# Performance work log

Hardware: AMD Instinct MI355X
Metric: run time of the kernel (lower is better)

## Reference

```python
import jax, jax.numpy as jnp
import numpy as np

B, C, D = 32768, 1000, 512
ALPHA, BETA = 1.0, 1.0
TEMPERATURE = 0.1


def setup_inputs() -> dict:
    key = jax.random.key(0)
    k1, k2, k3, k4 = jax.random.split(key, 4)
    return {
        "features_front": jax.random.normal(k1, (B, D), dtype=jnp.float32),
        "logits": jax.random.normal(k2, (B, C), dtype=jnp.float32),
        "labels": jax.random.randint(k3, (B,), 0, C, dtype=jnp.int64),
        "text_prototype": jax.random.normal(k4, (C, D), dtype=jnp.float32),
    }


def reference(features_front, logits, labels, text_prototype):
    num_class = text_prototype.shape[0]

    # F.cross_entropy (mean reduction)
    logp = jax.nn.log_softmax(logits, axis=-1)
    loss_ce = -jnp.mean(jnp.take_along_axis(logp, labels[:, None], axis=1)[:, 0])

    # F.normalize(prototypes, dim=1)
    norm = jnp.linalg.norm(text_prototype, axis=1, keepdims=True)
    prototypes = text_prototype / jnp.maximum(norm, 1e-12)

    # supervised contrastive term against class prototypes
    feat_dot_prototype = (features_front @ prototypes.T) / TEMPERATURE  # [B, C]
    logits_max = jax.lax.stop_gradient(jnp.max(feat_dot_prototype, axis=1, keepdims=True))
    lg = feat_dot_prototype - logits_max
    log_prob = lg - jnp.log(jnp.sum(jnp.exp(lg), axis=1, keepdims=True))
    mask = (labels[:, None] == jnp.arange(num_class)[None, :]).astype(log_prob.dtype)
    mean_log_prob_pos = jnp.sum(mask * log_prob, axis=1)
    simloss = -jnp.mean(mean_log_prob_pos)

    # prototype repulsion: sum_{i != j} exp(p_i . p_j) == masked exp-sum of Gram matrix
    gram = prototypes @ prototypes.T  # [C, C]
    offdiag = 1.0 - jnp.eye(num_class, dtype=gram.dtype)
    textloss = jnp.log(jnp.sum(jnp.exp(gram) * offdiag)) / num_class

    return ALPHA * simloss + BETA * loss_ce + textloss
```

## Files before the change

### kernel.cpp

```cpp
#include <hip/hip_runtime.h>
#include <math.h>

#define NB 32768
#define NC 1000
#define ND 512
#define NTILES 63
#define LOG2E 1.4426950408889634f
#define LN2 0.6931471805599453f
#define S2 14.426950408889634f
#define NBUCKET 64

typedef __attribute__((ext_vector_type(8))) short short8;
typedef __attribute__((ext_vector_type(4))) float f32x4;

__device__ __forceinline__ float fexp2(float x) {
    float r; asm("v_exp_f32 %0, %1" : "=v"(r) : "v"(x)); return r;
}
__device__ __forceinline__ float flog2(float x) {
    float r; asm("v_log_f32 %0, %1" : "=v"(r) : "v"(x)); return r;
}
__device__ __forceinline__ unsigned short bf16_rne(float f) {
    unsigned int u = __builtin_bit_cast(unsigned int, f);
    u += 0x7FFFu + ((u >> 16) & 1u);
    return (unsigned short)(u >> 16);
}
__device__ __forceinline__ short8 pack8f(float4 a, float4 b) {
    short8 s;
    s[0] = (short)bf16_rne(a.x); s[1] = (short)bf16_rne(a.y);
    s[2] = (short)bf16_rne(a.z); s[3] = (short)bf16_rne(a.w);
    s[4] = (short)bf16_rne(b.x); s[5] = (short)bf16_rne(b.y);
    s[6] = (short)bf16_rne(b.z); s[7] = (short)bf16_rne(b.w);
    return s;
}

__global__ __launch_bounds__(256) void norm_protos(const float* __restrict__ pro,
                                                   unsigned short* __restrict__ pbf) {
    const int row = blockIdx.x, t = threadIdx.x;
    const int tile = row >> 4, r = row & 15;
    const int kk = t >> 4, g = (t >> 2) & 3, slot = t & 3;
    unsigned int* dst = (unsigned int*)pbf +
        ((size_t)tile * 1024 + kk * 64 + g * 16 + r) * 4 + slot;
    if (row >= NC) { *dst = 0u; return; }
    const float* rp = pro + (size_t)row * ND;
    const float x0 = rp[2 * t], x1 = rp[2 * t + 1];
    float ss = x0 * x0 + x1 * x1;
#pragma unroll
    for (int o = 1; o < 64; o <<= 1) ss += __shfl_xor(ss, o, 64);
    __shared__ float part[4];
    if ((t & 63) == 0) part[t >> 6] = ss;
    __syncthreads();
    const float nrm = sqrtf(part[0] + part[1] + part[2] + part[3]);
    const float sc = 1.0f / fmaxf(nrm, 1e-12f);
    *dst = (unsigned int)bf16_rne(x0 * sc) | ((unsigned int)bf16_rne(x1 * sc) << 16);
}

__global__ __launch_bounds__(256, 3) void fat_kernel(const float* __restrict__ feat,
                                                     const float* __restrict__ logits,
                                                     const int* __restrict__ labels,
                                                     const unsigned short* __restrict__ pbf,
                                                     float* __restrict__ buckets,
                                                     float4* __restrict__ part) {
    __shared__ short8 lds[2][1024];
    __shared__ float wsum[4];
    const int role = blockIdx.x % 3;
    const int idx = blockIdx.x / 3;
    const int t = threadIdx.x;
    const int wid = t >> 6, lane = t & 63;
    const short8* frag = (const short8*)pbf;

    if (role == 0) {
        const int rb = idx >> 1, ch = idx & 1;
        const int t0 = ch ? 32 : 0;
        const int nt = ch ? 31 : 32;
        const int r16 = lane & 15, g = lane >> 4;
        const int rowbase = rb * 64 + wid * 16;

        {
            const short8* src = frag + t0 * 1024;
#pragma unroll
            for (int q = 0; q < 4; ++q) {
                const int id = t + 256 * q;
                __builtin_amdgcn_global_load_lds(
                    (const __attribute__((address_space(1))) unsigned int*)(src + id),
                    (__attribute__((address_space(3))) unsigned int*)(&lds[0][0] + id), 16, 0, 0);
            }
        }
        short8 bf[16];
        {
            const float* f0 = feat + (size_t)(rowbase + r16) * ND + 8 * g;
#pragma unroll
            for (int kk = 0; kk < 16; ++kk)
                bf[kk] = pack8f(*(const float4*)(f0 + 32 * kk), *(const float4*)(f0 + 32 * kk + 4));
        }
        int lab0 = labels[rowbase + r16];
        lab0 = lab0 < 0 ? 0 : (lab0 > NC - 1 ? NC - 1 : lab0);

        float m0 = -INFINITY, ls0 = 0.f, lv0 = 0.f;
        __syncthreads();

#pragma unroll 1
        for (int j = 0; j < nt; ++j) {
            const short8* cur = lds[j & 1];
            if (j + 1 < nt) {
                short8* nxt = lds[(j + 1) & 1];
                const short8* src = frag + (t0 + j + 1) * 1024;
#pragma unroll
                for (int q = 0; q < 4; ++q) {
                    const int id = t + 256 * q;
                    __builtin_amdgcn_global_load_lds(
                        (const __attribute__((address_space(1))) unsigned int*)(src + id),
                        (__attribute__((address_space(3))) unsigned int*)(nxt + id), 16, 0, 0);
                }
            }
            f32x4 aE = {0.f, 0.f, 0.f, 0.f}, aO = {0.f, 0.f, 0.f, 0.f};
#pragma unroll
            for (int kk = 0; kk < 8; ++kk) {
                aE = __builtin_amdgcn_mfma_f32_16x16x32_bf16(cur[kk * 64 + lane], bf[kk], aE, 0, 0, 0);
                aO = __builtin_amdgcn_mfma_f32_16x16x32_bf16(cur[(8 + kk) * 64 + lane], bf[8 + kk], aO, 0, 0, 0);
            }
            const int cbase = (t0 + j) * 16 + g * 4;
            float x[4];
#pragma unroll
            for (int rI = 0; rI < 4; ++rI) {
                const float v = (aE[rI] + aO[rI]) * S2;
                x[rI] = (cbase + rI < NC) ? v : -INFINITY;
                lv0 += (cbase + rI == lab0) ? v : 0.f;
            }
            const float tmax = fmaxf(fmaxf(x[0], x[1]), fmaxf(x[2], x[3]));
            const float mn = fmaxf(m0, tmax);
            ls0 *= fexp2(m0 - mn);
            m0 = mn;
            ls0 += fexp2(x[0] - mn) + fexp2(x[1] - mn) + fexp2(x[2] - mn) + fexp2(x[3] - mn);
            __syncthreads();
        }

#pragma unroll
        for (int o = 16; o <= 32; o <<= 1) {
            const float mo = __shfl_xor(m0, o, 64), lo = __shfl_xor(ls0, o, 64);
            lv0 += __shfl_xor(lv0, o, 64);
            const float mm = fmaxf(m0, mo);
            ls0 = ls0 * fexp2(m0 - mm) + lo * fexp2(mo - mm);
            m0 = mm;
        }
        if (lane < 16) {
            float4 p; p.x = m0; p.y = ls0; p.z = lv0; p.w = 0.f;
            part[(size_t)(rowbase + r16) * 2 + ch] = p;
        }

    } else if (role == 1) {
        const int rowbase = idx * 32 + wid * 8;
        const int q4 = lane >> 4, l16 = lane & 15;
        float localce = 0.f;
#pragma unroll 1
        for (int i = 0; i < 2; ++i) {
            const int row = rowbase + 4 * i + q4;
            const float* rp = logits + (size_t)row * NC;
            const float4* rp4 = (const float4*)rp;
            float4 xs[16];
#pragma unroll
            for (int j = 0; j < 15; ++j) {
                const float4 v = rp4[l16 + 16 * j];
                xs[j].x = v.x * LOG2E; xs[j].y = v.y * LOG2E;
                xs[j].z = v.z * LOG2E; xs[j].w = v.w * LOG2E;
            }
            if (l16 < 10) {
                const float4 v = rp4[l16 + 240];
                xs[15].x = v.x * LOG2E; xs[15].y = v.y * LOG2E;
                xs[15].z = v.z * LOG2E; xs[15].w = v.w * LOG2E;
            } else {
                xs[15].x = xs[15].y = xs[15].z = xs[15].w = -INFINITY;
            }
            float m = -INFINITY;
#pragma unroll
            for (int j = 0; j < 16; ++j)
                m = fmaxf(m, fmaxf(fmaxf(xs[j].x, xs[j].y), fmaxf(xs[j].z, xs[j].w)));
#pragma unroll
            for (int o = 1; o <= 8; o <<= 1) m = fmaxf(m, __shfl_xor(m, o, 64));
            float s = 0.f;
#pragma unroll
            for (int j = 0; j < 16; ++j)
                s += fexp2(xs[j].x - m) + fexp2(xs[j].y - m) +
                     fexp2(xs[j].z - m) + fexp2(xs[j].w - m);
#pragma unroll
            for (int o = 1; o <= 8; o <<= 1) s += __shfl_xor(s, o, 64);
            if (l16 == 0) {
                int lab = labels[row];
                lab = lab < 0 ? 0 : (lab > NC - 1 ? NC - 1 : lab);
                localce += (m + flog2(s)) * LN2 - rp[lab];
            }
        }
#pragma unroll
        for (int o = 1; o < 64; o <<= 1) localce += __shfl_xor(localce, o, 64);
        if (lane == 0) wsum[wid] = localce;
        __syncthreads();
        if (t == 0)
            atomicAdd(buckets + 1024 + (idx & (NBUCKET - 1)) * 16,
                      (wsum[0] + wsum[1] + wsum[2] + wsum[3]) * (1.0f / (float)NB));

    } else {
        if (idx >= 1008) return;
        const int ct = idx >> 4;
        const int bx = idx & 15;
        const int r16 = lane & 15, g = lane >> 4;
        const int btile = bx * 4 + wid;
        const int irow = btile * 16 + r16;

        short8 af[16], bfr[16];
#pragma unroll
        for (int kk = 0; kk < 16; ++kk) {
            af[kk] = frag[(size_t)ct * 1024 + kk * 64 + lane];
            bfr[kk] = frag[(size_t)btile * 1024 + kk * 64 + lane];
        }
        f32x4 dacc = {0.f, 0.f, 0.f, 0.f};
#pragma unroll
        for (int kk = 0; kk < 16; ++kk)
            dacc = __builtin_amdgcn_mfma_f32_16x16x32_bf16(af[kk], bfr[kk], dacc, 0, 0, 0);

        float s = 0.f;
        if (irow < NC) {
            const int cbase = ct * 16 + g * 4;
#pragma unroll
            for (int rI = 0; rI < 4; ++rI) {
                const int j = cbase + rI;
                if (j < NC && j != irow) s += fexp2(dacc[rI] * LOG2E);
            }
        }
#pragma unroll
        for (int o = 1; o < 64; o <<= 1) s += __shfl_xor(s, o, 64);
        if (lane == 0) wsum[wid] = s;
        __syncthreads();
        if (t == 0)
            atomicAdd(buckets + 2048 + (idx & (NBUCKET - 1)) * 16,
                      wsum[0] + wsum[1] + wsum[2] + wsum[3]);
    }
}

__global__ __launch_bounds__(256) void simmerge_kernel(const float4* __restrict__ part,
                                                       float* __restrict__ buckets) {
    __shared__ float wsum[4];
    const int t = threadIdx.x, wid = t >> 6, lane = t & 63;
    const int row = blockIdx.x * 256 + t;
    const float4 p0 = part[(size_t)row * 2];
    const float4 p1 = part[(size_t)row * 2 + 1];
    const float M = fmaxf(p0.x, p1.x);
    const float LS = p0.y * fexp2(p0.x - M) + p1.y * fexp2(p1.x - M);
    float v = (M + flog2(LS) - (p0.z + p1.z)) * LN2 * (1.0f / (float)NB);
#pragma unroll
    for (int o = 1; o < 64; o <<= 1) v += __shfl_xor(v, o, 64);
    if (lane == 0) wsum[wid] = v;
    __syncthreads();
    if (t == 0)
        atomicAdd(buckets + (blockIdx.x & (NBUCKET - 1)) * 16,
                  wsum[0] + wsum[1] + wsum[2] + wsum[3]);
}

__global__ void combine_kernel(const float* __restrict__ a, float* __restrict__ out) {
    const int t = threadIdx.x;
    float s = a[t * 16], c = a[1024 + t * 16], gr = a[2048 + t * 16];
#pragma unroll
    for (int o = 1; o < 64; o <<= 1) {
        s += __shfl_xor(s, o, 64);
        c += __shfl_xor(c, o, 64);
        gr += __shfl_xor(gr, o, 64);
    }
    if (t == 0) out[0] = s + c + logf(gr) * (1.0f / (float)NC);
}

extern "C" void kernel_launch(void* const* d_in, const int* in_sizes, int n_in,
                              void* d_out, int out_size, void* d_ws, size_t ws_size,
                              hipStream_t stream) {
    const float* feat   = (const float*)d_in[0];
    const float* logits = (const float*)d_in[1];
    const int*   labels = (const int*)d_in[2];
    const float* pro    = (const float*)d_in[3];
    float* out = (float*)d_out;

    float* acc = (float*)d_ws;
    unsigned short* pbf = (unsigned short*)((char*)d_ws + 16384);
    float4* part = (float4*)((char*)d_ws + (2u << 20));

    hipMemsetAsync(d_ws, 0, 3072 * sizeof(float), stream);
    hipLaunchKernelGGL(norm_protos,     dim3(1024), dim3(256), 0, stream, pro, pbf);
    hipLaunchKernelGGL(fat_kernel,      dim3(3072), dim3(256), 0, stream,
                       feat, logits, labels, pbf, acc, part);
    hipLaunchKernelGGL(simmerge_kernel, dim3(128),  dim3(256), 0, stream, part, acc);
    hipLaunchKernelGGL(combine_kernel,  dim3(1),    dim3(64),  0, stream, acc, out);
}
```

Measured before the change: 99.05 us.

## Double rows per wave in sim GEMM and rebalance block role mix

Each sim-role wave now processes two 16-row feature tiles against each staged prototype tile, reusing every LDS fragment for two MFMAs and halving the number of sim blocks. The block role split changes from thirds to fifths so the CE and Gram roles keep their counts, and the grid shrinks to match. The CE path folds the LOG2E scaling into an FMA inside the exp. Launch bounds drop to one block per SIMD target, which allows many more registers but may reduce occupancy and latency hiding.

```diff
diff --git a/kernel.cpp b/kernel.cpp
--- a/kernel.cpp
+++ b/kernel.cpp
@@ -54,7 +54,7 @@
     *dst = (unsigned int)bf16_rne(x0 * sc) | ((unsigned int)bf16_rne(x1 * sc) << 16);
 }
 
-__global__ __launch_bounds__(256, 3) void fat_kernel(const float* __restrict__ feat,
+__global__ __launch_bounds__(256, 1) void fat_kernel(const float* __restrict__ feat,
                                                      const float* __restrict__ logits,
                                                      const int* __restrict__ labels,
                                                      const unsigned short* __restrict__ pbf,
@@ -62,18 +62,19 @@
                                                      float4* __restrict__ part) {
     __shared__ short8 lds[2][1024];
     __shared__ float wsum[4];
-    const int role = blockIdx.x % 3;
-    const int idx = blockIdx.x / 3;
+    const int r5 = blockIdx.x % 5;
+    const int q5 = blockIdx.x / 5;
     const int t = threadIdx.x;
     const int wid = t >> 6, lane = t & 63;
     const short8* frag = (const short8*)pbf;
 
-    if (role == 0) {
+    if (r5 == 0) {
+        const int idx = q5;
         const int rb = idx >> 1, ch = idx & 1;
         const int t0 = ch ? 32 : 0;
         const int nt = ch ? 31 : 32;
         const int r16 = lane & 15, g = lane >> 4;
-        const int rowbase = rb * 64 + wid * 16;
+        const int rowbase = rb * 128 + wid * 32;
 
         {
             const short8* src = frag + t0 * 1024;
@@ -85,17 +86,23 @@
                     (__attribute__((address_space(3))) unsigned int*)(&lds[0][0] + id), 16, 0, 0);
             }
         }
-        short8 bf[16];
+        short8 bf0[16], bf1[16];
         {
             const float* f0 = feat + (size_t)(rowbase + r16) * ND + 8 * g;
-#pragma unroll
-            for (int kk = 0; kk < 16; ++kk)
-                bf[kk] = pack8f(*(const float4*)(f0 + 32 * kk), *(const float4*)(f0 + 32 * kk + 4));
+            const float* f1 = f0 + 16 * ND;
+#pragma unroll
+            for (int kk = 0; kk < 16; ++kk) {
+                bf0[kk] = pack8f(*(const float4*)(f0 + 32 * kk), *(const float4*)(f0 + 32 * kk + 4));
+                bf1[kk] = pack8f(*(const float4*)(f1 + 32 * kk), *(const float4*)(f1 + 32 * kk + 4));
+            }
         }
         int lab0 = labels[rowbase + r16];
+        int lab1 = labels[rowbase + 16 + r16];
         lab0 = lab0 < 0 ? 0 : (lab0 > NC - 1 ? NC - 1 : lab0);
+        lab1 = lab1 < 0 ? 0 : (lab1 > NC - 1 ? NC - 1 : lab1);
 
         float m0 = -INFINITY, ls0 = 0.f, lv0 = 0.f;
+        float m1 = -INFINITY, ls1 = 0.f, lv1 = 0.f;
         __syncthreads();
 
 #pragma unroll 1
@@ -112,42 +119,76 @@
                         (__attribute__((address_space(3))) unsigned int*)(nxt + id), 16, 0, 0);
                 }
             }
-            f32x4 aE = {0.f, 0.f, 0.f, 0.f}, aO = {0.f, 0.f, 0.f, 0.f};
+            f32x4 e0 = {0.f, 0.f, 0.f, 0.f}, o0 = {0.f, 0.f, 0.f, 0.f};
+            f32x4 e1 = {0.f, 0.f, 0.f, 0.f}, o1 = {0.f, 0.f, 0.f, 0.f};
 #pragma unroll
             for (int kk = 0; kk < 8; ++kk) {
-                aE = __builtin_amdgcn_mfma_f32_16x16x32_bf16(cur[kk * 64 + lane], bf[kk], aE, 0, 0, 0);
-                aO = __builtin_amdgcn_mfma_f32_16x16x32_bf16(cur[(8 + kk) * 64 + lane], bf[8 + kk], aO, 0, 0, 0);
+                const short8 A = cur[kk * 64 + lane];
+                const short8 A2 = cur[(8 + kk) * 64 + lane];
+                e0 = __builtin_amdgcn_mfma_f32_16x16x32_bf16(A, bf0[kk], e0, 0, 0, 0);
+                o0 = __builtin_amdgcn_mfma_f32_16x16x32_bf16(A2, bf0[8 + kk], o0, 0, 0, 0);
+                e1 = __builtin_amdgcn_mfma_f32_16x16x32_bf16(A, bf1[kk], e1, 0, 0, 0);
+                o1 = __builtin_amdgcn_mfma_f32_16x16x32_bf16(A2, bf1[8 + kk], o1, 0, 0, 0);
             }
             const int cbase = (t0 + j) * 16 + g * 4;
-            float x[4];
-#pragma unroll
-            for (int rI = 0; rI < 4; ++rI) {
-                const float v = (aE[rI] + aO[rI]) * S2;
-                x[rI] = (cbase + rI < NC) ? v : -INFINITY;
-                lv0 += (cbase + rI == lab0) ? v : 0.f;
-            }
-            const float tmax = fmaxf(fmaxf(x[0], x[1]), fmaxf(x[2], x[3]));
-            const float mn = fmaxf(m0, tmax);
-            ls0 *= fexp2(m0 - mn);
-            m0 = mn;
-            ls0 += fexp2(x[0] - mn) + fexp2(x[1] - mn) + fexp2(x[2] - mn) + fexp2(x[3] - mn);
+            {
+                float x[4];
+#pragma unroll
+                for (int rI = 0; rI < 4; ++rI) {
+                    const float v = (e0[rI] + o0[rI]) * S2;
+                    x[rI] = (cbase + rI < NC) ? v : -INFINITY;
+                    lv0 += (cbase + rI == lab0) ? v : 0.f;
+                }
+                const float tmax = fmaxf(fmaxf(x[0], x[1]), fmaxf(x[2], x[3]));
+                const float mn = fmaxf(m0, tmax);
+                ls0 *= fexp2(m0 - mn);
+                m0 = mn;
+                ls0 += fexp2(x[0] - mn) + fexp2(x[1] - mn) + fexp2(x[2] - mn) + fexp2(x[3] - mn);
+            }
+            {
+                float x[4];
+#pragma unroll
+                for (int rI = 0; rI < 4; ++rI) {
+                    const float v = (e1[rI] + o1[rI]) * S2;
+                    x[rI] = (cbase + rI < NC) ? v : -INFINITY;
+                    lv1 += (cbase + rI == lab1) ? v : 0.f;
+                }
+                const float tmax = fmaxf(fmaxf(x[0], x[1]), fmaxf(x[2], x[3]));
+                const float mn = fmaxf(m1, tmax);
+                ls1 *= fexp2(m1 - mn);
+                m1 = mn;
+                ls1 += fexp2(x[0] - mn) + fexp2(x[1] - mn) + fexp2(x[2] - mn) + fexp2(x[3] - mn);
+            }
             __syncthreads();
         }
 
 #pragma unroll
         for (int o = 16; o <= 32; o <<= 1) {
-            const float mo = __shfl_xor(m0, o, 64), lo = __shfl_xor(ls0, o, 64);
-            lv0 += __shfl_xor(lv0, o, 64);
-            const float mm = fmaxf(m0, mo);
-            ls0 = ls0 * fexp2(m0 - mm) + lo * fexp2(mo - mm);
-            m0 = mm;
+            {
+                const float mo = __shfl_xor(m0, o, 64), lo = __shfl_xor(ls0, o, 64);
+                lv0 += __shfl_xor(lv0, o, 64);
+                const float mm = fmaxf(m0, mo);
+                ls0 = ls0 * fexp2(m0 - mm) + lo * fexp2(mo - mm);
+                m0 = mm;
+            }
+            {
+                const float mo = __shfl_xor(m1, o, 64), lo = __shfl_xor(ls1, o, 64);
+                lv1 += __shfl_xor(lv1, o, 64);
+                const float mm = fmaxf(m1, mo);
+                ls1 = ls1 * fexp2(m1 - mm) + lo * fexp2(mo - mm);
+                m1 = mm;
+            }
         }
         if (lane < 16) {
             float4 p; p.x = m0; p.y = ls0; p.z = lv0; p.w = 0.f;
             part[(size_t)(rowbase + r16) * 2 + ch] = p;
-        }
-
-    } else if (role == 1) {
+        } else if (lane < 32) {
+            float4 p; p.x = m1; p.y = ls1; p.z = lv1; p.w = 0.f;
+            part[(size_t)(rowbase + 16 + r16) * 2 + ch] = p;
+        }
+
+    } else if (r5 == 1 || r5 == 3) {
+        const int idx = q5 * 2 + (r5 == 3);
         const int rowbase = idx * 32 + wid * 8;
         const int q4 = lane >> 4, l16 = lane & 15;
         float localce = 0.f;
@@ -158,15 +199,9 @@
             const float4* rp4 = (const float4*)rp;
             float4 xs[16];
 #pragma unroll
-            for (int j = 0; j < 15; ++j) {
-                const float4 v = rp4[l16 + 16 * j];
-                xs[j].x = v.x * LOG2E; xs[j].y = v.y * LOG2E;
-                xs[j].z = v.z * LOG2E; xs[j].w = v.w * LOG2E;
-            }
+            for (int j = 0; j < 15; ++j) xs[j] = rp4[l16 + 16 * j];
             if (l16 < 10) {
-                const float4 v = rp4[l16 + 240];
-                xs[15].x = v.x * LOG2E; xs[15].y = v.y * LOG2E;
-                xs[15].z = v.z * LOG2E; xs[15].w = v.w * LOG2E;
+                xs[15] = rp4[l16 + 240];
             } else {
                 xs[15].x = xs[15].y = xs[15].z = xs[15].w = -INFINITY;
             }
@@ -176,17 +211,18 @@
                 m = fmaxf(m, fmaxf(fmaxf(xs[j].x, xs[j].y), fmaxf(xs[j].z, xs[j].w)));
 #pragma unroll
             for (int o = 1; o <= 8; o <<= 1) m = fmaxf(m, __shfl_xor(m, o, 64));
+            const float m2 = m * LOG2E;
             float s = 0.f;
 #pragma unroll
             for (int j = 0; j < 16; ++j)
-                s += fexp2(xs[j].x - m) + fexp2(xs[j].y - m) +
-                     fexp2(xs[j].z - m) + fexp2(xs[j].w - m);
+                s += fexp2(fmaf(xs[j].x, LOG2E, -m2)) + fexp2(fmaf(xs[j].y, LOG2E, -m2)) +
+                     fexp2(fmaf(xs[j].z, LOG2E, -m2)) + fexp2(fmaf(xs[j].w, LOG2E, -m2));
 #pragma unroll
             for (int o = 1; o <= 8; o <<= 1) s += __shfl_xor(s, o, 64);
             if (l16 == 0) {
                 int lab = labels[row];
                 lab = lab < 0 ? 0 : (lab > NC - 1 ? NC - 1 : lab);
-                localce += (m + flog2(s)) * LN2 - rp[lab];
+                localce += (m2 + flog2(s)) * LN2 - rp[lab];
             }
         }
 #pragma unroll
@@ -198,6 +234,7 @@
                       (wsum[0] + wsum[1] + wsum[2] + wsum[3]) * (1.0f / (float)NB));
 
     } else {
+        const int idx = q5 * 2 + (r5 == 4);
         if (idx >= 1008) return;
         const int ct = idx >> 4;
         const int bx = idx & 15;
@@ -281,7 +318,7 @@
 
     hipMemsetAsync(d_ws, 0, 3072 * sizeof(float), stream);
     hipLaunchKernelGGL(norm_protos,     dim3(1024), dim3(256), 0, stream, pro, pbf);
-    hipLaunchKernelGGL(fat_kernel,      dim3(3072), dim3(256), 0, stream,
+    hipLaunchKernelGGL(fat_kernel,      dim3(2560), dim3(256), 0, stream,
                        feat, logits, labels, pbf, acc, part);
     hipLaunchKernelGGL(simmerge_kernel, dim3(128),  dim3(256), 0, stream, part, acc);
     hipLaunchKernelGGL(combine_kernel,  dim3(1),    dim3(64),  0, stream, acc, out);
```

After: 137.3 us. 1.39x slower.
